# Kernel tuning notes

Hardware: AMD Instinct MI355X
Metric: run time of the kernel (lower is better)

The kernel has to match this reference:

```python
import jax, jax.numpy as jnp
import numpy as np

N = 50000      # num_nodes
R = 90         # num_relations
E = 800000     # num_edges
H = 16         # hidden channels
B = 30         # num_bases
C = 8          # num_classes


def setup_inputs() -> dict:
    key = jax.random.key(0)
    ks = jax.random.split(key, 10)
    edge_index = jax.random.randint(ks[0], (2, E), 0, N, dtype=jnp.int64)
    edge_type = jax.random.randint(ks[1], (E,), 0, R, dtype=jnp.int64)
    s1 = 1.0 / np.sqrt(N)
    s2 = 1.0 / np.sqrt(H)
    return {
        "edge_index": edge_index,
        "edge_type": edge_type,
        # layer 1: in=N (featureless one-hot), out=H
        "basis1": jax.random.normal(ks[2], (B, N, H), jnp.float32) * s1,
        "comp1": jax.random.normal(ks[3], (R, B), jnp.float32) * (1.0 / np.sqrt(B)),
        "root1": jax.random.normal(ks[4], (N, H), jnp.float32) * s1,
        "bias1": jnp.zeros((H,), jnp.float32),
        # layer 2: in=H, out=C
        "basis2": jax.random.normal(ks[5], (B, H, C), jnp.float32) * s2,
        "comp2": jax.random.normal(ks[6], (R, B), jnp.float32) * (1.0 / np.sqrt(B)),
        "root2": jax.random.normal(ks[7], (H, C), jnp.float32) * s2,
        "bias2": jnp.zeros((C,), jnp.float32),
    }


def reference(edge_index, edge_type, basis1, comp1, root1, bias1,
              basis2, comp2, root2, bias2):
    src, dst = edge_index[0], edge_index[1]
    # per-(dst, relation) degree -> mean aggregation per relation (PyG RGCNConv aggr='mean')
    seg = dst * R + edge_type                      # [E]
    deg = jax.ops.segment_sum(jnp.ones((E,), jnp.float32), seg, num_segments=N * R)
    inv_deg = jnp.where(deg > 0, 1.0 / jnp.maximum(deg, 1.0), 0.0)
    norm = inv_deg[seg][:, None]                   # [E, 1]

    # ---- layer 1 (x = None -> one-hot node features; message = W_r[src]) ----
    W1 = jnp.einsum('rb,bnh->rnh', comp1, basis1)  # [R, N, H]
    m1 = W1[edge_type, src] * norm                 # [E, H]
    h = jax.ops.segment_sum(m1, dst, num_segments=N) + root1 + bias1  # [N, H]
    h = jax.nn.relu(h)

    # ---- layer 2 ----
    W2 = jnp.einsum('rb,bhc->rhc', comp2, basis2)  # [R, H, C]
    m2 = jnp.einsum('eh,ehc->ec', h[src], W2[edge_type]) * norm       # [E, C]
    out = jax.ops.segment_sum(m2, dst, num_segments=N) + h @ root2 + bias2
    return jax.nn.log_softmax(out, axis=1)
```

## Files before the change

kernel.cpp:

```cpp
#include <hip/hip_runtime.h>

#define NNODES 50000
#define NREL   90
#define NEDGE  800000
#define HDIM   16
#define NBASIS 30
#define NCLS   8
#define NPART  392
#define CH     4096
#define P1BLK  ((NEDGE + CH - 1) / CH)
#define CAPSTG 2816
#define GS     16
#define BSTR2  260
#define CROW2  20

typedef __fp16 h2 __attribute__((ext_vector_type(2)));

static __device__ __forceinline__ unsigned pk2(float a, float b) {
    h2 p = __builtin_amdgcn_cvt_pkrtz(a, b);
    return __builtin_bit_cast(unsigned, p);
}
static __device__ __forceinline__ h2 uph(unsigned u) {
    return __builtin_bit_cast(h2, u);
}
static __device__ __forceinline__ float fd2(unsigned a, unsigned b, float c) {
#if __has_builtin(__builtin_amdgcn_fdot2)
    return __builtin_amdgcn_fdot2(uph(a), uph(b), c, false);
#else
    h2 x = uph(a), y = uph(b);
    return fmaf((float)x.y, (float)y.y, fmaf((float)x.x, (float)y.x, c));
#endif
}

__device__ __forceinline__ void scan512_incl(int* sc) {
    int t = threadIdx.x;
#pragma unroll
    for (int d = 1; d < 512; d <<= 1) {
        int v0 = sc[t];
        int a0 = (t >= d) ? sc[t - d] : 0;
        int v1 = sc[t + 256];
        int a1 = sc[t + 256 - d];
        __syncthreads();
        sc[t] = v0 + a0;
        sc[t + 256] = v1 + a1;
        __syncthreads();
    }
}

__device__ __forceinline__ void scan128_incl(int* sc) {
    int t = threadIdx.x;
#pragma unroll
    for (int d = 1; d < 128; d <<= 1) {
        int v = 0, a = 0;
        if (t < 128) { v = sc[t]; a = (t >= d) ? sc[t - d] : 0; }
        __syncthreads();
        if (t < 128) sc[t] = v + a;
        __syncthreads();
    }
}

__global__ __launch_bounds__(256) void initc_kernel(int* __restrict__ gcur_s,
                                                    int* __restrict__ gcur_d,
                                                    int* __restrict__ gcnt,
                                                    const float* __restrict__ comp1,
                                                    unsigned* __restrict__ comp_pk) {
    int t = blockIdx.x * 256 + threadIdx.x;
    if (t < NPART) { gcur_s[t] = t * CAPSTG; gcur_d[t] = t * CAPSTG; }
    else if (t == NPART) { gcnt[0] = 0; gcnt[1] = 0; }
    int i = t - 512;
    if (i >= 0 && i < NREL * 15) {
        int r = i / 15;
        int b2 = i - r * 15;
        comp_pk[r * CROW2 + b2] = pk2(comp1[r * NBASIS + 2 * b2],
                                      comp1[r * NBASIS + 2 * b2 + 1]);
    }
    if (i >= NREL * 15 && i < NREL * 15 + NREL * (CROW2 - 15)) {
        int j = i - NREL * 15;
        int r = j / (CROW2 - 15);
        int pcol = 15 + (j - r * (CROW2 - 15));
        comp_pk[r * CROW2 + pcol] = 0;
    }
}

__global__ __launch_bounds__(256) void p1d_kernel(const int* __restrict__ ei,
                                                  const int* __restrict__ et,
                                                  int* __restrict__ gcur_d,
                                                  int2* __restrict__ stg_d) {
    __shared__ int2 sorted[CH];
    __shared__ int hist[NPART], loff[NPART], cur[NPART], gbase[NPART];
    __shared__ int sc[512];
    int base = blockIdx.x * CH;
    int nitems = min(CH, NEDGE - base);
    int t = threadIdx.x;
    for (int i = t; i < NPART; i += 256) hist[i] = 0;
    __syncthreads();
    for (int i = t; i < nitems; i += 256)
        atomicAdd(&hist[ei[NEDGE + base + i] >> 7], 1);
    __syncthreads();
    sc[t]       = (t < NPART) ? hist[t] : 0;
    sc[t + 256] = (t + 256 < NPART) ? hist[t + 256] : 0;
    __syncthreads();
    scan512_incl(sc);
    for (int p = t; p < NPART; p += 256) {
        int lo = p ? sc[p - 1] : 0;
        loff[p] = lo;
        cur[p] = lo;
        if (hist[p]) gbase[p] = atomicAdd(&gcur_d[p], hist[p]);
    }
    __syncthreads();
    for (int i = t; i < nitems; i += 256) {
        int e = base + i;
        int src = ei[e], dst = ei[NEDGE + e], r = et[e];
        int rk = atomicAdd(&cur[dst >> 7], 1);
        sorted[rk] = make_int2(src | (r << 16), dst);
    }
    __syncthreads();
    for (int s = t; s < nitems; s += 256) {
        int2 it = sorted[s];
        int p = it.y >> 7;
        stg_d[gbase[p] + (s - loff[p])] = it;
    }
}

__global__ __launch_bounds__(256) void p2d_kernel(const int* __restrict__ gcur_d,
                                                  const int2* __restrict__ stg_d,
                                                  int* __restrict__ gcur_s,
                                                  int2* __restrict__ stg_s,
                                                  int* __restrict__ gcnt,
                                                  int* __restrict__ d_sr,
                                                  float* __restrict__ d_norm,
                                                  int* __restrict__ offs_d,
                                                  int* __restrict__ cnt_d) {
    __shared__ int2 sorted[CAPSTG];
    __shared__ int2 sorted2[CAPSTG];
    __shared__ int h[128], off[128], cur[128];
    __shared__ int sc[512];
    __shared__ int shist[NPART], sloff[NPART], scur[NPART], sgbase[NPART];
    __shared__ int kb;
    int p = blockIdx.x;
    int base = p * CAPSTG;
    int n = min(gcur_d[p] - base, CAPSTG);
    int t = threadIdx.x;
    if (t < 128) h[t] = 0;
    __syncthreads();
    for (int s = t; s < n; s += 256)
        atomicAdd(&h[stg_d[base + s].y & 127], 1);
    __syncthreads();
    if (t < 128) sc[t] = h[t];
    __syncthreads();
    scan128_incl(sc);
    if (t < 128) { int lo = t ? sc[t - 1] : 0; off[t] = lo; cur[t] = lo; }
    if (t == 0) kb = atomicAdd(&gcnt[0], n);
    __syncthreads();
    for (int s = t; s < n; s += 256) {
        int2 it = stg_d[base + s];
        int rk = atomicAdd(&cur[it.y & 127], 1);
        sorted[rk] = it;
    }
    __syncthreads();
    int kbase = kb;
    for (int s = t; s < n; s += 256) {
        int2 it = sorted[s];
        int key = it.y & 127;
        int r = it.x >> 16;
        int o = off[key], oe = o + h[key];
        int c = 0;
        for (int kk = o; kk < oe; ++kk)
            c += ((sorted[kk].x >> 16) == r);
        d_sr[kbase + s] = it.x;
        d_norm[kbase + s] = 1.0f / (float)c;
    }
    if (t < 128) {
        int node = (p << 7) + t;
        if (node < NNODES) { offs_d[node] = kbase + off[t]; cnt_d[node] = h[t]; }
    }
    for (int i = t; i < NPART; i += 256) shist[i] = 0;
    __syncthreads();
    for (int s = t; s < n; s += 256)
        atomicAdd(&shist[(sorted[s].x & 0xFFFF) >> 7], 1);
    __syncthreads();
    sc[t]       = (t < NPART) ? shist[t] : 0;
    sc[t + 256] = (t + 256 < NPART) ? shist[t + 256] : 0;
    __syncthreads();
    scan512_incl(sc);
    for (int pp = t; pp < NPART; pp += 256) {
        int lo = pp ? sc[pp - 1] : 0;
        sloff[pp] = lo;
        scur[pp] = lo;
        if (shist[pp]) sgbase[pp] = atomicAdd(&gcur_s[pp], shist[pp]);
    }
    __syncthreads();
    for (int s = t; s < n; s += 256) {
        int2 it = sorted[s];
        int rk = atomicAdd(&scur[(it.x & 0xFFFF) >> 7], 1);
        sorted2[rk] = make_int2(it.x, kbase + s);
    }
    __syncthreads();
    for (int s = t; s < n; s += 256) {
        int2 it = sorted2[s];
        int pp = (it.x & 0xFFFF) >> 7;
        stg_s[sgbase[pp] + (s - sloff[pp])] = it;
    }
}

__global__ __launch_bounds__(256) void p2s_kernel(const int* __restrict__ gcur_s,
                                                  const int2* __restrict__ stg_s,
                                                  int* __restrict__ gcnt,
                                                  int* __restrict__ sB,
                                                  int* __restrict__ s_k,
                                                  int* __restrict__ offs_s,
                                                  int* __restrict__ cnt_s) {
    __shared__ int2 sorted[CAPSTG];
    __shared__ int h[128], off[128], cur[128], sc[128];
    __shared__ int jb;
    int p = blockIdx.x;
    int base = p * CAPSTG;
    int n = min(gcur_s[p] - base, CAPSTG);
    int t = threadIdx.x;
    if (t < 128) h[t] = 0;
    __syncthreads();
    for (int s = t; s < n; s += 256)
        atomicAdd(&h[stg_s[base + s].x & 127], 1);
    __syncthreads();
    if (t < 128) sc[t] = h[t];
    __syncthreads();
    scan128_incl(sc);
    if (t < 128) { int lo = t ? sc[t - 1] : 0; off[t] = lo; cur[t] = lo; }
    if (t == 0) jb = atomicAdd(&gcnt[1], n);
    __syncthreads();
    for (int s = t; s < n; s += 256) {
        int2 it = stg_s[base + s];
        int rk = atomicAdd(&cur[it.x & 127], 1);
        sorted[rk] = it;
    }
    __syncthreads();
    int jbase = jb;
    for (int s = t; s < n; s += 256) {
        int2 it = sorted[s];
        sB[jbase + s]  = it.x;
        s_k[jbase + s] = it.y;
    }
    if (t < 128) {
        int node = (p << 7) + t;
        if (node < NNODES) { offs_s[node] = jbase + off[t]; cnt_s[node] = h[t]; }
    }
}

__global__ __launch_bounds__(256) void msg1_lds(const float* __restrict__ basis1,
                                                const unsigned* __restrict__ comp_pk,
                                                const int* __restrict__ offs_s,
                                                const int* __restrict__ cnt_s,
                                                const int* __restrict__ sB,
                                                const int* __restrict__ s_k,
                                                unsigned* __restrict__ m1) {
    __shared__ unsigned bspk[GS * BSTR2];
    __shared__ unsigned cpk[NREL * CROW2];
    int src0 = blockIdx.x * GS;
    int t = threadIdx.x;
    for (int i = t; i < (NREL * CROW2) / 4; i += 256)
        ((uint4*)cpk)[i] = ((const uint4*)comp_pk)[i];
    for (int i4 = t; i4 < 15 * 64; i4 += 256) {
        int b2 = i4 >> 6;
        int w  = i4 & 63;
        const float4* bp = (const float4*)basis1;
        float4 a = bp[(size_t)(2 * b2)     * (NNODES * 4) + (size_t)src0 * 4 + w];
        float4 b = bp[(size_t)(2 * b2 + 1) * (NNODES * 4) + (size_t)src0 * 4 + w];
        int s = w >> 2, q = w & 3;
        uint4 o;
        o.x = pk2(a.x, b.x);
        o.y = pk2(a.y, b.y);
        o.z = pk2(a.z, b.z);
        o.w = pk2(a.w, b.w);
        *((uint4*)(bspk + s * BSTR2 + b2 * 16 + q * 4)) = o;
    }
    __syncthreads();
    int n0 = offs_s[src0];
    int lastS = src0 + GS - 1;
    int n1 = offs_s[lastS] + cnt_s[lastS];
    int end = n1 * 4;
    for (int ii = n0 * 4 + t; ii < end; ii += 512) {
        int iiB = ii + 256;
        bool hasB = iiB < end;
        int jA = ii >> 2, qA = ii & 3;
        int pkA = sB[jA];
        int kA  = s_k[jA];
        const uint4* crowA = (const uint4*)(cpk + (pkA >> 16) * CROW2);
        const unsigned* bwA = bspk + ((pkA & 0xFFFF) - src0) * BSTR2 + qA * 4;
        uint4 cA0 = crowA[0], cA1 = crowA[1], cA2 = crowA[2], cA3 = crowA[3];
        int jB = hasB ? (iiB >> 2) : jA;
        int qB = iiB & 3;
        int pkB = sB[jB];
        int kB  = s_k[jB];
        const uint4* crowB = (const uint4*)(cpk + (pkB >> 16) * CROW2);
        const unsigned* bwB = bspk + ((pkB & 0xFFFF) - src0) * BSTR2 + qB * 4;
        uint4 cB0 = crowB[0], cB1 = crowB[1], cB2 = crowB[2], cB3 = crowB[3];
        float a0 = 0.f, a1 = 0.f, a2 = 0.f, a3 = 0.f;
        float b0 = 0.f, b1 = 0.f, b2_ = 0.f, b3 = 0.f;
#define MSG1_STEP2(B2, CA, CB) { \
        uint4 vA = *((const uint4*)(bwA + (B2) * 16)); \
        uint4 vB = *((const uint4*)(bwB + (B2) * 16)); \
        a0 = fd2(vA.x, (CA), a0);  b0 = fd2(vB.x, (CB), b0); \
        a1 = fd2(vA.y, (CA), a1);  b1 = fd2(vB.y, (CB), b1); \
        a2 = fd2(vA.z, (CA), a2);  b2_ = fd2(vB.z, (CB), b2_); \
        a3 = fd2(vA.w, (CA), a3);  b3 = fd2(vB.w, (CB), b3); }
        MSG1_STEP2(0,  cA0.x, cB0.x) MSG1_STEP2(1,  cA0.y, cB0.y)
        MSG1_STEP2(2,  cA0.z, cB0.z) MSG1_STEP2(3,  cA0.w, cB0.w)
        MSG1_STEP2(4,  cA1.x, cB1.x) MSG1_STEP2(5,  cA1.y, cB1.y)
        MSG1_STEP2(6,  cA1.z, cB1.z) MSG1_STEP2(7,  cA1.w, cB1.w)
        MSG1_STEP2(8,  cA2.x, cB2.x) MSG1_STEP2(9,  cA2.y, cB2.y)
        MSG1_STEP2(10, cA2.z, cB2.z) MSG1_STEP2(11, cA2.w, cB2.w)
        MSG1_STEP2(12, cA3.x, cB3.x) MSG1_STEP2(13, cA3.y, cB3.y)
        MSG1_STEP2(14, cA3.z, cB3.z)
#undef MSG1_STEP2
        ((uint2*)m1)[(size_t)kA * 4 + qA] = make_uint2(pk2(a0, a1), pk2(a2, a3));
        if (hasB)
            ((uint2*)m1)[(size_t)kB * 4 + qB] = make_uint2(pk2(b0, b1), pk2(b2_, b3));
    }
}

__global__ __launch_bounds__(256) void gather1_flat(const unsigned* __restrict__ m1,
                                                    const float* __restrict__ d_norm,
                                                    const int* __restrict__ offs_d,
                                                    const int* __restrict__ cnt_d,
                                                    const float* __restrict__ root1,
                                                    const float* __restrict__ bias1,
                                                    float* __restrict__ h) {
    int idx = blockIdx.x * blockDim.x + threadIdx.x;
    if (idx >= NNODES * 4) return;
    int dst = idx >> 2;
    int q   = idx & 3;
    int k0 = offs_d[dst];
    int k1 = k0 + cnt_d[dst];
    float4 acc = make_float4(0.f, 0.f, 0.f, 0.f);
    for (int k = k0; k < k1; ++k) {
        uint2 v = ((const uint2*)m1)[(size_t)k * 4 + q];
        float nm = d_norm[k];
        h2 x = uph(v.x), y = uph(v.y);
        acc.x = fmaf(nm, (float)x.x, acc.x);
        acc.y = fmaf(nm, (float)x.y, acc.y);
        acc.z = fmaf(nm, (float)y.x, acc.z);
        acc.w = fmaf(nm, (float)y.y, acc.w);
    }
    float4 rt = ((const float4*)root1)[idx];
    float4 bi = ((const float4*)bias1)[q];
    float4 o;
    o.x = fmaxf(acc.x + rt.x + bi.x, 0.f);
    o.y = fmaxf(acc.y + rt.y + bi.y, 0.f);
    o.z = fmaxf(acc.z + rt.z + bi.z, 0.f);
    o.w = fmaxf(acc.w + rt.w + bi.w, 0.f);
    ((float4*)h)[idx] = o;
}

__global__ __launch_bounds__(256) void w2_kernel(const float* __restrict__ basis2,
                                                 const float* __restrict__ comp2,
                                                 const float* __restrict__ root2,
                                                 float* __restrict__ w2t,
                                                 float* __restrict__ r2t) {
    int i = blockIdx.x * blockDim.x + threadIdx.x;
    if (i >= NREL * HDIM * NCLS) return;
    int kk = i & (HDIM - 1);
    int c  = (i >> 4) & (NCLS - 1);
    int r  = i >> 7;
    float acc = 0.f;
#pragma unroll
    for (int b = 0; b < NBASIS; ++b)
        acc += comp2[r * NBASIS + b] * basis2[(b * HDIM + kk) * NCLS + c];
    w2t[i] = acc;
    if (i < HDIM * NCLS) {
        int c2 = i >> 4;
        int k2 = i & (HDIM - 1);
        r2t[i] = root2[k2 * NCLS + c2];
    }
}

__global__ __launch_bounds__(256) void msg2_kernel(const float* __restrict__ h,
                                                   const float* __restrict__ w2t,
                                                   const int* __restrict__ d_sr,
                                                   const float* __restrict__ d_norm,
                                                   float* __restrict__ m2) {
    int idx = blockIdx.x * blockDim.x + threadIdx.x;
    int k = idx >> 3;
    int c = idx & (NCLS - 1);
    int pk = d_sr[k];
    float nm = d_norm[k];
    int src = pk & 0xFFFF;
    int r   = pk >> 16;
    const float4* __restrict__ hp = (const float4*)h + src * 4;
    const float4* __restrict__ wp = (const float4*)w2t + (r * NCLS + c) * 4;
    float a = 0.f;
#pragma unroll
    for (int qq = 0; qq < 4; ++qq) {
        float4 hv = hp[qq];
        float4 wv = wp[qq];
        a = fmaf(hv.x, wv.x, a);
        a = fmaf(hv.y, wv.y, a);
        a = fmaf(hv.z, wv.z, a);
        a = fmaf(hv.w, wv.w, a);
    }
    m2[idx] = nm * a;
}

__global__ __launch_bounds__(256) void gather2_kernel(const float* __restrict__ m2,
                                                      const float* __restrict__ h,
                                                      const float* __restrict__ r2t,
                                                      const int* __restrict__ offs_d,
                                                      const int* __restrict__ cnt_d,
                                                      const float* __restrict__ bias2,
                                                      float* __restrict__ out) {
    int idx = blockIdx.x * blockDim.x + threadIdx.x;
    if (idx >= NNODES * NCLS) return;
    int dst = idx >> 3;
    int c   = idx & (NCLS - 1);
    int k0 = offs_d[dst];
    int k1 = k0 + cnt_d[dst];
    float acc = 0.f;
    for (int k = k0; k < k1; ++k)
        acc += m2[k * NCLS + c];
    float v = acc + bias2[c];
    const float4* __restrict__ hd = (const float4*)h + dst * 4;
    const float4* __restrict__ rp = (const float4*)r2t + c * 4;
#pragma unroll
    for (int qq = 0; qq < 4; ++qq) {
        float4 hv = hd[qq];
        float4 rv = rp[qq];
        v = fmaf(hv.x, rv.x, v);
        v = fmaf(hv.y, rv.y, v);
        v = fmaf(hv.z, rv.z, v);
        v = fmaf(hv.w, rv.w, v);
    }
    float mx = v;
    mx = fmaxf(mx, __shfl_xor(mx, 1));
    mx = fmaxf(mx, __shfl_xor(mx, 2));
    mx = fmaxf(mx, __shfl_xor(mx, 4));
    float s = expf(v - mx);
    s += __shfl_xor(s, 1);
    s += __shfl_xor(s, 2);
    s += __shfl_xor(s, 4);
    out[idx] = v - mx - logf(s);
}

__global__ __launch_bounds__(256) void degcnt_fb(const int* __restrict__ ei,
                                                 const int* __restrict__ et,
                                                 int* __restrict__ deg) {
    int e = blockIdx.x * blockDim.x + threadIdx.x;
    if (e >= NEDGE) return;
    atomicAdd(&deg[ei[NEDGE + e] * NREL + et[e]], 1);
}

__global__ __launch_bounds__(256) void layer1_flat(const int* __restrict__ ei,
                                                   const int* __restrict__ et,
                                                   const float* __restrict__ basis1,
                                                   const float* __restrict__ comp1,
                                                   const int* __restrict__ deg,
                                                   float* __restrict__ h) {
    long long idx = (long long)blockIdx.x * blockDim.x + threadIdx.x;
    if (idx >= (long long)NEDGE * HDIM) return;
    int e  = (int)(idx >> 4);
    int hh = (int)(idx & (HDIM - 1));
    int src = ei[e];
    int dst = ei[NEDGE + e];
    int r   = et[e];
    float norm = 1.0f / (float)deg[dst * NREL + r];
    const float* __restrict__ cp = comp1 + r * NBASIS;
    float acc = 0.f;
#pragma unroll
    for (int b = 0; b < NBASIS; ++b)
        acc += cp[b] * basis1[(b * NNODES + src) * HDIM + hh];
    atomicAdd(&h[dst * HDIM + hh], norm * acc);
}

__global__ __launch_bounds__(256) void relu_kernel(float* __restrict__ h,
                                                   const float* __restrict__ root1,
                                                   const float* __restrict__ bias1) {
    int i = blockIdx.x * blockDim.x + threadIdx.x;
    if (i >= NNODES * HDIM) return;
    float v = h[i] + root1[i] + bias1[i & (HDIM - 1)];
    h[i] = v > 0.f ? v : 0.f;
}

__global__ __launch_bounds__(256) void layer2_flat(const int* __restrict__ ei,
                                                   const int* __restrict__ et,
                                                   const float* __restrict__ h,
                                                   const float* __restrict__ w2t,
                                                   const int* __restrict__ deg,
                                                   float* __restrict__ out_tmp) {
    long long idx = (long long)blockIdx.x * blockDim.x + threadIdx.x;
    if (idx >= (long long)NEDGE * NCLS) return;
    int e = (int)(idx >> 3);
    int c = (int)(idx & (NCLS - 1));
    int src = ei[e];
    int dst = ei[NEDGE + e];
    int r   = et[e];
    float norm = 1.0f / (float)deg[dst * NREL + r];
    const float4* __restrict__ hp = (const float4*)h + src * 4;
    const float4* __restrict__ wp = (const float4*)w2t + (r * NCLS + c) * 4;
    float a = 0.f;
#pragma unroll
    for (int qq = 0; qq < 4; ++qq) {
        float4 hv = hp[qq];
        float4 wv = wp[qq];
        a = fmaf(hv.x, wv.x, a);
        a = fmaf(hv.y, wv.y, a);
        a = fmaf(hv.z, wv.z, a);
        a = fmaf(hv.w, wv.w, a);
    }
    atomicAdd(&out_tmp[dst * NCLS + c], norm * a);
}

__global__ __launch_bounds__(256) void final_kernel(const float* __restrict__ out_tmp,
                                                    const float* __restrict__ h,
                                                    const float* __restrict__ root2,
                                                    const float* __restrict__ bias2,
                                                    float* __restrict__ out) {
    int n = blockIdx.x * blockDim.x + threadIdx.x;
    if (n >= NNODES) return;
    float hv[HDIM];
#pragma unroll
    for (int i = 0; i < HDIM; ++i) hv[i] = h[n * HDIM + i];
    float v[NCLS];
    float mx = -1e30f;
#pragma unroll
    for (int c = 0; c < NCLS; ++c) {
        float acc = out_tmp[n * NCLS + c] + bias2[c];
#pragma unroll
        for (int i = 0; i < HDIM; ++i) acc += hv[i] * root2[i * NCLS + c];
        v[c] = acc;
        mx = fmaxf(mx, acc);
    }
    float s = 0.f;
#pragma unroll
    for (int c = 0; c < NCLS; ++c) s += expf(v[c] - mx);
    float ls = logf(s);
#pragma unroll
    for (int c = 0; c < NCLS; ++c) out[n * NCLS + c] = v[c] - mx - ls;
}

extern "C" void kernel_launch(void* const* d_in, const int* in_sizes, int n_in,
                              void* d_out, int out_size, void* d_ws, size_t ws_size,
                              hipStream_t stream) {
    const int*   ei     = (const int*)d_in[0];
    const int*   et     = (const int*)d_in[1];
    const float* basis1 = (const float*)d_in[2];
    const float* comp1  = (const float*)d_in[3];
    const float* root1  = (const float*)d_in[4];
    const float* bias1  = (const float*)d_in[5];
    const float* basis2 = (const float*)d_in[6];
    const float* comp2  = (const float*)d_in[7];
    const float* root2  = (const float*)d_in[8];
    const float* bias2  = (const float*)d_in[9];
    float* out = (float*)d_out;

    int*      gcur_s  = (int*)d_ws;
    int*      gcur_d  = gcur_s + NPART;
    int*      gcnt    = gcur_d + NPART;
    unsigned* comp_pk = (unsigned*)(gcnt + 4);
    int2*  stg_d  = (int2*)(comp_pk + NREL * CROW2);
    int2*  stg_s  = stg_d + (size_t)NPART * CAPSTG;
    int*   d_sr   = (int*)(stg_s + (size_t)NPART * CAPSTG);
    float* d_norm = (float*)(d_sr + NEDGE);
    int*   sB     = (int*)(d_norm + NEDGE);
    int*   s_k    = sB + NEDGE;
    int*   offs_s = s_k + NEDGE;
    int*   cnt_s  = offs_s + NNODES;
    int*   offs_d = cnt_s + NNODES;
    int*   cnt_d  = offs_d + NNODES;
    unsigned* m1  = (unsigned*)(cnt_d + NNODES);
    float* m2     = (float*)m1;
    float* h      = (float*)(m1 + (size_t)NEDGE * 8);
    float* w2t    = h + (size_t)NNODES * HDIM;
    float* r2t    = w2t + (size_t)NREL * HDIM * NCLS;
    size_t total_words = 2 * (size_t)NPART + 4 + NREL * CROW2 +
                         4 * (size_t)NPART * CAPSTG +
                         4 * (size_t)NEDGE + 4 * (size_t)NNODES +
                         (size_t)NEDGE * 8 + (size_t)NNODES * HDIM +
                         (size_t)NREL * HDIM * NCLS + HDIM * NCLS;

    if (ws_size >= total_words * sizeof(float)) {
        initc_kernel<<<8, 256, 0, stream>>>(gcur_s, gcur_d, gcnt, comp1, comp_pk);
        p1d_kernel<<<P1BLK, 256, 0, stream>>>(ei, et, gcur_d, stg_d);
        p2d_kernel<<<NPART - 1, 256, 0, stream>>>(gcur_d, stg_d, gcur_s, stg_s, gcnt,
                                                  d_sr, d_norm, offs_d, cnt_d);
        p2s_kernel<<<NPART - 1, 256, 0, stream>>>(gcur_s, stg_s, gcnt, sB, s_k, offs_s, cnt_s);

        msg1_lds<<<NNODES / GS, 256, 0, stream>>>(basis1, comp_pk, offs_s, cnt_s, sB, s_k, m1);
        gather1_flat<<<(NNODES * 4 + 255) / 256, 256, 0, stream>>>(
            m1, d_norm, offs_d, cnt_d, root1, bias1, h);
        w2_kernel<<<(NREL * HDIM * NCLS + 255) / 256, 256, 0, stream>>>(basis2, comp2, root2,
                                                                        w2t, r2t);
        msg2_kernel<<<(NEDGE * NCLS) / 256, 256, 0, stream>>>(h, w2t, d_sr, d_norm, m2);
        gather2_kernel<<<(NNODES * NCLS + 255) / 256, 256, 0, stream>>>(
            m2, h, r2t, offs_d, cnt_d, bias2, out);
        return;
    }

    {
        int*   deg_f   = (int*)d_ws;
        float* h_f     = (float*)(deg_f + (size_t)NNODES * NREL);
        float* out_tmp = h_f + (size_t)NNODES * HDIM;
        size_t zw = (size_t)NNODES * NREL + NNODES * HDIM + NNODES * NCLS;
        float* w2t_f   = out_tmp + (size_t)NNODES * NCLS;
        float* r2t_f   = w2t_f + (size_t)NREL * HDIM * NCLS;

        (void)hipMemsetAsync(d_ws, 0, zw * sizeof(float), stream);
        degcnt_fb<<<(NEDGE + 255) / 256, 256, 0, stream>>>(ei, et, deg_f);
        layer1_flat<<<((size_t)NEDGE * HDIM + 255) / 256, 256, 0, stream>>>(
            ei, et, basis1, comp1, deg_f, h_f);
        relu_kernel<<<(NNODES * HDIM + 255) / 256, 256, 0, stream>>>(h_f, root1, bias1);
        w2_kernel<<<(NREL * HDIM * NCLS + 255) / 256, 256, 0, stream>>>(basis2, comp2, root2,
                                                                        w2t_f, r2t_f);
        layer2_flat<<<((size_t)NEDGE * NCLS + 255) / 256, 256, 0, stream>>>(
            ei, et, h_f, w2t_f, deg_f, out_tmp);
        final_kernel<<<(NNODES + 255) / 256, 256, 0, stream>>>(out_tmp, h_f, root2, bias2, out);
    }
}
```

Measured before the change: 173.9 us.

## Reorder edge sorting to src-first so msg1 writes coalesced and gather1 scatters

The two-pass partition sort now buckets by source first and by destination second, the reverse of the old order. msg1 therefore writes its per-edge messages contiguously in source order, and the src-sorted index list is staged in LDS. The random indirection moves into gather1, which now reads m1 through a d_j index array. This trades scattered writes in msg1 for scattered reads in gather1, and adds a binary search per item in the p2s scatter. It also leaves a dead loop in p2s and packs the local dst id into the high bits of the key word.

New measurement: 187.4 us. 1.08x slower.

```diff
diff --git a/kernel.cpp b/kernel.cpp
--- a/kernel.cpp
+++ b/kernel.cpp
@@ -13,6 +13,7 @@
 #define GS     16
 #define BSTR2  260
 #define CROW2  20
+#define SBLCAP 1024
 
 typedef __fp16 h2 __attribute__((ext_vector_type(2)));
 
@@ -82,10 +83,10 @@
     }
 }
 
-__global__ __launch_bounds__(256) void p1d_kernel(const int* __restrict__ ei,
+__global__ __launch_bounds__(256) void p1s_kernel(const int* __restrict__ ei,
                                                   const int* __restrict__ et,
-                                                  int* __restrict__ gcur_d,
-                                                  int2* __restrict__ stg_d) {
+                                                  int* __restrict__ gcur_s,
+                                                  int2* __restrict__ stg_s) {
     __shared__ int2 sorted[CH];
     __shared__ int hist[NPART], loff[NPART], cur[NPART], gbase[NPART];
     __shared__ int sc[512];
@@ -95,7 +96,7 @@
     for (int i = t; i < NPART; i += 256) hist[i] = 0;
     __syncthreads();
     for (int i = t; i < nitems; i += 256)
-        atomicAdd(&hist[ei[NEDGE + base + i] >> 7], 1);
+        atomicAdd(&hist[ei[base + i] >> 7], 1);
     __syncthreads();
     sc[t]       = (t < NPART) ? hist[t] : 0;
     sc[t + 256] = (t + 256 < NPART) ? hist[t + 256] : 0;
@@ -105,37 +106,119 @@
         int lo = p ? sc[p - 1] : 0;
         loff[p] = lo;
         cur[p] = lo;
-        if (hist[p]) gbase[p] = atomicAdd(&gcur_d[p], hist[p]);
+        if (hist[p]) gbase[p] = atomicAdd(&gcur_s[p], hist[p]);
     }
     __syncthreads();
     for (int i = t; i < nitems; i += 256) {
         int e = base + i;
         int src = ei[e], dst = ei[NEDGE + e], r = et[e];
-        int rk = atomicAdd(&cur[dst >> 7], 1);
-        sorted[rk] = make_int2(src | (r << 16), dst);
+        int rk = atomicAdd(&cur[src >> 7], 1);
+        sorted[rk] = make_int2(dst | (r << 16), src);
     }
     __syncthreads();
     for (int s = t; s < nitems; s += 256) {
         int2 it = sorted[s];
         int p = it.y >> 7;
-        stg_d[gbase[p] + (s - loff[p])] = it;
-    }
-}
-
-__global__ __launch_bounds__(256) void p2d_kernel(const int* __restrict__ gcur_d,
-                                                  const int2* __restrict__ stg_d,
-                                                  int* __restrict__ gcur_s,
-                                                  int2* __restrict__ stg_s,
+        stg_s[gbase[p] + (s - loff[p])] = it;
+    }
+}
+
+__global__ __launch_bounds__(256) void p2s_kernel(const int* __restrict__ gcur_s,
+                                                  const int2* __restrict__ stg_s,
+                                                  int* __restrict__ gcur_d,
+                                                  int2* __restrict__ stg_d,
                                                   int* __restrict__ gcnt,
-                                                  int* __restrict__ d_sr,
-                                                  float* __restrict__ d_norm,
-                                                  int* __restrict__ offs_d,
-                                                  int* __restrict__ cnt_d) {
+                                                  int* __restrict__ sB,
+                                                  int* __restrict__ offs_s,
+                                                  int* __restrict__ cnt_s) {
     __shared__ int2 sorted[CAPSTG];
     __shared__ int2 sorted2[CAPSTG];
     __shared__ int h[128], off[128], cur[128];
     __shared__ int sc[512];
     __shared__ int shist[NPART], sloff[NPART], scur[NPART], sgbase[NPART];
+    __shared__ int jb;
+    int p = blockIdx.x;
+    int base = p * CAPSTG;
+    int n = min(gcur_s[p] - base, CAPSTG);
+    int t = threadIdx.x;
+    if (t < 128) h[t] = 0;
+    __syncthreads();
+    for (int s = t; s < n; s += 256)
+        atomicAdd(&h[stg_s[base + s].y & 127], 1);
+    __syncthreads();
+    if (t < 128) sc[t] = h[t];
+    __syncthreads();
+    scan128_incl(sc);
+    if (t < 128) { int lo = t ? sc[t - 1] : 0; off[t] = lo; cur[t] = lo; }
+    if (t == 0) jb = atomicAdd(&gcnt[0], n);
+    __syncthreads();
+    for (int s = t; s < n; s += 256) {
+        int2 it = stg_s[base + s];
+        int rk = atomicAdd(&cur[it.y & 127], 1);
+        sorted[rk] = it;
+    }
+    __syncthreads();
+    int jbase = jb;
+    for (int s = t; s < n; s += 256) {
+        int2 it = sorted[s];
+        int r = it.x >> 16;
+        sB[jbase + s] = it.y | (r << 16);
+    }
+    if (t < 128) {
+        int node = (p << 7) + t;
+        if (node < NNODES) { offs_s[node] = jbase + off[t]; cnt_s[node] = h[t]; }
+    }
+    for (int i = t; i < NPART; i += 256) shist[i] = 0;
+    __syncthreads();
+    for (int s = t; s < n; s += 256)
+        atomicAdd(&shist[(sorted[s].x & 0xFFFF) >> 7], 1);
+    __syncthreads();
+    sc[t]       = (t < NPART) ? shist[t] : 0;
+    sc[t + 256] = (t + 256 < NPART) ? shist[t + 256] : 0;
+    __syncthreads();
+    scan512_incl(sc);
+    for (int pp = t; pp < NPART; pp += 256) {
+        int lo = pp ? sc[pp - 1] : 0;
+        sloff[pp] = lo;
+        scur[pp] = lo;
+        if (shist[pp]) sgbase[pp] = atomicAdd(&gcur_d[pp], shist[pp]);
+    }
+    __syncthreads();
+    for (int s = t; s < n; s += 256) {
+        int2 it = sorted[s];
+        int dst = it.x & 0xFFFF;
+        int r   = it.x >> 16;
+        int rk = atomicAdd(&scur[dst >> 7], 1);
+        sorted2[rk] = make_int2(it.y | (r << 16) | ((dst & 127) << 23), jbase + s);
+    }
+    __syncthreads();
+    for (int s = t; s < n; s += 256) {
+        int2 it = sorted2[s];
+        int pp = ((it.x & 0xFFFF) >> 7);
+        (void)pp;
+    }
+    for (int s = t; s < n; s += 256) {
+        int2 it = sorted2[s];
+        int lo = 0, hi = NPART - 1;
+        while (lo < hi) {
+            int mid = (lo + hi) >> 1;
+            if (sc[mid] > s) hi = mid; else lo = mid + 1;
+        }
+        int P = lo;
+        stg_d[sgbase[P] + (s - sloff[P])] = it;
+    }
+}
+
+__global__ __launch_bounds__(256) void p2d_kernel(const int* __restrict__ gcur_d,
+                                                  const int2* __restrict__ stg_d,
+                                                  int* __restrict__ gcnt,
+                                                  int* __restrict__ d_sr,
+                                                  int* __restrict__ d_j,
+                                                  float* __restrict__ d_norm,
+                                                  int* __restrict__ offs_d,
+                                                  int* __restrict__ cnt_d) {
+    __shared__ int2 sorted[CAPSTG];
+    __shared__ int h[128], off[128], cur[128], sc[128];
     __shared__ int kb;
     int p = blockIdx.x;
     int base = p * CAPSTG;
@@ -144,105 +227,36 @@
     if (t < 128) h[t] = 0;
     __syncthreads();
     for (int s = t; s < n; s += 256)
-        atomicAdd(&h[stg_d[base + s].y & 127], 1);
+        atomicAdd(&h[(stg_d[base + s].x >> 23) & 127], 1);
     __syncthreads();
     if (t < 128) sc[t] = h[t];
     __syncthreads();
     scan128_incl(sc);
     if (t < 128) { int lo = t ? sc[t - 1] : 0; off[t] = lo; cur[t] = lo; }
-    if (t == 0) kb = atomicAdd(&gcnt[0], n);
+    if (t == 0) kb = atomicAdd(&gcnt[1], n);
     __syncthreads();
     for (int s = t; s < n; s += 256) {
         int2 it = stg_d[base + s];
-        int rk = atomicAdd(&cur[it.y & 127], 1);
+        int rk = atomicAdd(&cur[(it.x >> 23) & 127], 1);
         sorted[rk] = it;
     }
     __syncthreads();
     int kbase = kb;
     for (int s = t; s < n; s += 256) {
         int2 it = sorted[s];
-        int key = it.y & 127;
-        int r = it.x >> 16;
+        int key = (it.x >> 23) & 127;
+        int r = (it.x >> 16) & 127;
         int o = off[key], oe = o + h[key];
         int c = 0;
         for (int kk = o; kk < oe; ++kk)
-            c += ((sorted[kk].x >> 16) == r);
-        d_sr[kbase + s] = it.x;
+            c += (((sorted[kk].x >> 16) & 127) == r);
+        d_sr[kbase + s]   = it.x & 0x7FFFFF;
+        d_j[kbase + s]    = it.y;
         d_norm[kbase + s] = 1.0f / (float)c;
     }
     if (t < 128) {
         int node = (p << 7) + t;
         if (node < NNODES) { offs_d[node] = kbase + off[t]; cnt_d[node] = h[t]; }
-    }
-    for (int i = t; i < NPART; i += 256) shist[i] = 0;
-    __syncthreads();
-    for (int s = t; s < n; s += 256)
-        atomicAdd(&shist[(sorted[s].x & 0xFFFF) >> 7], 1);
-    __syncthreads();
-    sc[t]       = (t < NPART) ? shist[t] : 0;
-    sc[t + 256] = (t + 256 < NPART) ? shist[t + 256] : 0;
-    __syncthreads();
-    scan512_incl(sc);
-    for (int pp = t; pp < NPART; pp += 256) {
-        int lo = pp ? sc[pp - 1] : 0;
-        sloff[pp] = lo;
-        scur[pp] = lo;
-        if (shist[pp]) sgbase[pp] = atomicAdd(&gcur_s[pp], shist[pp]);
-    }
-    __syncthreads();
-    for (int s = t; s < n; s += 256) {
-        int2 it = sorted[s];
-        int rk = atomicAdd(&scur[(it.x & 0xFFFF) >> 7], 1);
-        sorted2[rk] = make_int2(it.x, kbase + s);
-    }
-    __syncthreads();
-    for (int s = t; s < n; s += 256) {
-        int2 it = sorted2[s];
-        int pp = (it.x & 0xFFFF) >> 7;
-        stg_s[sgbase[pp] + (s - sloff[pp])] = it;
-    }
-}
-
-__global__ __launch_bounds__(256) void p2s_kernel(const int* __restrict__ gcur_s,
-                                                  const int2* __restrict__ stg_s,
-                                                  int* __restrict__ gcnt,
-                                                  int* __restrict__ sB,
-                                                  int* __restrict__ s_k,
-                                                  int* __restrict__ offs_s,
-                                                  int* __restrict__ cnt_s) {
-    __shared__ int2 sorted[CAPSTG];
-    __shared__ int h[128], off[128], cur[128], sc[128];
-    __shared__ int jb;
-    int p = blockIdx.x;
-    int base = p * CAPSTG;
-    int n = min(gcur_s[p] - base, CAPSTG);
-    int t = threadIdx.x;
-    if (t < 128) h[t] = 0;
-    __syncthreads();
-    for (int s = t; s < n; s += 256)
-        atomicAdd(&h[stg_s[base + s].x & 127], 1);
-    __syncthreads();
-    if (t < 128) sc[t] = h[t];
-    __syncthreads();
-    scan128_incl(sc);
-    if (t < 128) { int lo = t ? sc[t - 1] : 0; off[t] = lo; cur[t] = lo; }
-    if (t == 0) jb = atomicAdd(&gcnt[1], n);
-    __syncthreads();
-    for (int s = t; s < n; s += 256) {
-        int2 it = stg_s[base + s];
-        int rk = atomicAdd(&cur[it.x & 127], 1);
-        sorted[rk] = it;
-    }
-    __syncthreads();
-    int jbase = jb;
-    for (int s = t; s < n; s += 256) {
-        int2 it = sorted[s];
-        sB[jbase + s]  = it.x;
-        s_k[jbase + s] = it.y;
-    }
-    if (t < 128) {
-        int node = (p << 7) + t;
-        if (node < NNODES) { offs_s[node] = jbase + off[t]; cnt_s[node] = h[t]; }
     }
 }
 
@@ -251,10 +265,10 @@
                                                 const int* __restrict__ offs_s,
                                                 const int* __restrict__ cnt_s,
                                                 const int* __restrict__ sB,
-                                                const int* __restrict__ s_k,
                                                 unsigned* __restrict__ m1) {
     __shared__ unsigned bspk[GS * BSTR2];
     __shared__ unsigned cpk[NREL * CROW2];
+    __shared__ int sbl[SBLCAP];
     int src0 = blockIdx.x * GS;
     int t = threadIdx.x;
     for (int i = t; i < (NREL * CROW2) / 4; i += 256)
@@ -273,24 +287,26 @@
         o.w = pk2(a.w, b.w);
         *((uint4*)(bspk + s * BSTR2 + b2 * 16 + q * 4)) = o;
     }
-    __syncthreads();
     int n0 = offs_s[src0];
     int lastS = src0 + GS - 1;
     int n1 = offs_s[lastS] + cnt_s[lastS];
+    for (int i = n0 + t; i < n1 && (i - n0) < SBLCAP; i += 256)
+        sbl[i - n0] = sB[i];
+    __syncthreads();
     int end = n1 * 4;
     for (int ii = n0 * 4 + t; ii < end; ii += 512) {
         int iiB = ii + 256;
         bool hasB = iiB < end;
         int jA = ii >> 2, qA = ii & 3;
-        int pkA = sB[jA];
-        int kA  = s_k[jA];
+        int oA = jA - n0;
+        int pkA = (oA < SBLCAP) ? sbl[oA] : sB[jA];
         const uint4* crowA = (const uint4*)(cpk + (pkA >> 16) * CROW2);
         const unsigned* bwA = bspk + ((pkA & 0xFFFF) - src0) * BSTR2 + qA * 4;
         uint4 cA0 = crowA[0], cA1 = crowA[1], cA2 = crowA[2], cA3 = crowA[3];
         int jB = hasB ? (iiB >> 2) : jA;
         int qB = iiB & 3;
-        int pkB = sB[jB];
-        int kB  = s_k[jB];
+        int oB = jB - n0;
+        int pkB = (oB < SBLCAP) ? sbl[oB] : sB[jB];
         const uint4* crowB = (const uint4*)(cpk + (pkB >> 16) * CROW2);
         const unsigned* bwB = bspk + ((pkB & 0xFFFF) - src0) * BSTR2 + qB * 4;
         uint4 cB0 = crowB[0], cB1 = crowB[1], cB2 = crowB[2], cB3 = crowB[3];
@@ -312,13 +328,14 @@
         MSG1_STEP2(12, cA3.x, cB3.x) MSG1_STEP2(13, cA3.y, cB3.y)
         MSG1_STEP2(14, cA3.z, cB3.z)
 #undef MSG1_STEP2
-        ((uint2*)m1)[(size_t)kA * 4 + qA] = make_uint2(pk2(a0, a1), pk2(a2, a3));
+        ((uint2*)m1)[(size_t)jA * 4 + qA] = make_uint2(pk2(a0, a1), pk2(a2, a3));
         if (hasB)
-            ((uint2*)m1)[(size_t)kB * 4 + qB] = make_uint2(pk2(b0, b1), pk2(b2_, b3));
+            ((uint2*)m1)[(size_t)jB * 4 + qB] = make_uint2(pk2(b0, b1), pk2(b2_, b3));
     }
 }
 
 __global__ __launch_bounds__(256) void gather1_flat(const unsigned* __restrict__ m1,
+                                                    const int* __restrict__ d_j,
                                                     const float* __restrict__ d_norm,
                                                     const int* __restrict__ offs_d,
                                                     const int* __restrict__ cnt_d,
@@ -333,7 +350,8 @@
     int k1 = k0 + cnt_d[dst];
     float4 acc = make_float4(0.f, 0.f, 0.f, 0.f);
     for (int k = k0; k < k1; ++k) {
-        uint2 v = ((const uint2*)m1)[(size_t)k * 4 + q];
+        int j = d_j[k];
+        uint2 v = ((const uint2*)m1)[(size_t)j * 4 + q];
         float nm = d_norm[k];
         h2 x = uph(v.x), y = uph(v.y);
         acc.x = fmaf(nm, (float)x.x, acc.x);
@@ -554,13 +572,13 @@
     int*      gcur_d  = gcur_s + NPART;
     int*      gcnt    = gcur_d + NPART;
     unsigned* comp_pk = (unsigned*)(gcnt + 4);
-    int2*  stg_d  = (int2*)(comp_pk + NREL * CROW2);
-    int2*  stg_s  = stg_d + (size_t)NPART * CAPSTG;
-    int*   d_sr   = (int*)(stg_s + (size_t)NPART * CAPSTG);
+    int2*  stg_s  = (int2*)(comp_pk + NREL * CROW2);
+    int2*  stg_d  = stg_s + (size_t)NPART * CAPSTG;
+    int*   d_sr   = (int*)(stg_d + (size_t)NPART * CAPSTG);
     float* d_norm = (float*)(d_sr + NEDGE);
     int*   sB     = (int*)(d_norm + NEDGE);
-    int*   s_k    = sB + NEDGE;
-    int*   offs_s = s_k + NEDGE;
+    int*   d_j    = sB + NEDGE;
+    int*   offs_s = d_j + NEDGE;
     int*   cnt_s  = offs_s + NNODES;
     int*   offs_d = cnt_s + NNODES;
     int*   cnt_d  = offs_d + NNODES;
@@ -577,14 +595,15 @@
 
     if (ws_size >= total_words * sizeof(float)) {
         initc_kernel<<<8, 256, 0, stream>>>(gcur_s, gcur_d, gcnt, comp1, comp_pk);
-        p1d_kernel<<<P1BLK, 256, 0, stream>>>(ei, et, gcur_d, stg_d);
-        p2d_kernel<<<NPART - 1, 256, 0, stream>>>(gcur_d, stg_d, gcur_s, stg_s, gcnt,
-                                                  d_sr, d_norm, offs_d, cnt_d);
-        p2s_kernel<<<NPART - 1, 256, 0, stream>>>(gcur_s, stg_s, gcnt, sB, s_k, offs_s, cnt_s);
-
-        msg1_lds<<<NNODES / GS, 256, 0, stream>>>(basis1, comp_pk, offs_s, cnt_s, sB, s_k, m1);
+        p1s_kernel<<<P1BLK, 256, 0, stream>>>(ei, et, gcur_s, stg_s);
+        p2s_kernel<<<NPART - 1, 256, 0, stream>>>(gcur_s, stg_s, gcur_d, stg_d, gcnt,
+                                                  sB, offs_s, cnt_s);
+        p2d_kernel<<<NPART - 1, 256, 0, stream>>>(gcur_d, stg_d, gcnt,
+                                                  d_sr, d_j, d_norm, offs_d, cnt_d);
+
+        msg1_lds<<<NNODES / GS, 256, 0, stream>>>(basis1, comp_pk, offs_s, cnt_s, sB, m1);
         gather1_flat<<<(NNODES * 4 + 255) / 256, 256, 0, stream>>>(
-            m1, d_norm, offs_d, cnt_d, root1, bias1, h);
+            m1, d_j, d_norm, offs_d, cnt_d, root1, bias1, h);
         w2_kernel<<<(NREL * HDIM * NCLS + 255) / 256, 256, 0, stream>>>(basis2, comp2, root2,
                                                                         w2t, r2t);
         msg2_kernel<<<(NEDGE * NCLS) / 256, 256, 0, stream>>>(h, w2t, d_sr, d_norm, m2);
```
